# Performance work log

Measured on AMD Instinct MI355X. Metric: run time of the kernel, lower is better.

The kernel has to match this reference:

```python
import jax, jax.numpy as jnp
import numpy as np

N = 50000   # nodes
E = 600000  # edges
IN = 128    # in_channels
H = 128     # hidden
G = 64      # graphs in batch


def setup_inputs() -> dict:
    key = jax.random.key(0)
    ks = jax.random.split(key, 12)
    x = jax.random.normal(ks[0], (N, IN), jnp.float32)
    edge_index = jax.random.randint(ks[1], (2, E), 0, N, dtype=jnp.int64)
    batch = jnp.sort(jax.random.randint(ks[2], (N,), 0, G, dtype=jnp.int64))

    def glorot(k, i, o):
        return jax.random.normal(k, (i, o), jnp.float32) / np.float32(np.sqrt(i))

    return {
        "x": x, "edge_index": edge_index, "batch": batch,
        "W1": glorot(ks[3], IN, H), "b1": jnp.zeros((H,), jnp.float32),
        "W2": glorot(ks[4], H, H),  "b2": jnp.zeros((H,), jnp.float32),
        "W3": glorot(ks[5], H, H),  "b3": jnp.zeros((H,), jnp.float32),
        "Wl": glorot(ks[6], H, 2),  "bl": jnp.zeros((2,), jnp.float32),
    }


def gcn_conv(x, W, b, src, dst, n):
    # PyG GCNConv: linear transform, add self-loops, symmetric deg^-1/2 norm, scatter-add.
    h = x @ W                                   # [n, H]
    loop = jnp.arange(n, dtype=src.dtype)
    s = jnp.concatenate([src, loop])            # [E+n]
    d = jnp.concatenate([dst, loop])
    deg = jax.ops.segment_sum(jnp.ones_like(d, jnp.float32), d, num_segments=n)
    dinv = jax.lax.rsqrt(deg)                   # deg >= 1 thanks to self-loops
    norm = dinv[s] * dinv[d]                    # [E+n]
    out = jax.ops.segment_sum(h[s] * norm[:, None], d, num_segments=n)
    return out + b


def reference(x, edge_index, batch, W1, b1, W2, b2, W3, b3, Wl, bl):
    src, dst = edge_index[0], edge_index[1]
    h = jax.nn.relu(gcn_conv(x, W1, b1, src, dst, N))
    h = jax.nn.relu(gcn_conv(h, W2, b2, src, dst, N))
    h = jax.nn.relu(gcn_conv(h, W3, b3, src, dst, N))
    # global_mean_pool over graph ids
    cnt = jax.ops.segment_sum(jnp.ones((N,), jnp.float32), batch, num_segments=G)
    pooled = jax.ops.segment_sum(h, batch, num_segments=G) / jnp.maximum(cnt, 1.0)[:, None]
    # dropout is identity in eval mode
    return pooled @ Wl + bl                     # [G, 2]
```

## Files before the change

kernel.cpp:

```cpp
#include <hip/hip_runtime.h>


#define THREADS 256
#define ELLW 48
#define ELLS 64

typedef __attribute__((ext_vector_type(8))) short short8;
typedef __attribute__((ext_vector_type(4))) float f32x4;

__device__ inline unsigned short bf16_1(float a) {
    unsigned u = __float_as_uint(a);
    u += 0x7FFF + ((u >> 16) & 1);
    return (unsigned short)(u >> 16);
}
__device__ inline void bf16_split(float f, unsigned short& hi, unsigned short& lo) {
    unsigned u = __float_as_uint(f);
    unsigned r = u + 0x7FFF + ((u >> 16) & 1);
    hi = (unsigned short)(r >> 16);
    float hf = __uint_as_float((unsigned)hi << 16);
    float lf = f - hf;
    unsigned ul = __float_as_uint(lf);
    lo = (unsigned short)((ul + 0x7FFF + ((ul >> 16) & 1)) >> 16);
}

__global__ __launch_bounds__(THREADS) void zero_cnt_k(int* __restrict__ ell, int n) {
    int i = blockIdx.x * THREADS + threadIdx.x;
    if (i < n) ell[(size_t)i * ELLS] = 0;
}

__global__ __launch_bounds__(THREADS) void ell_fill_k(const int* __restrict__ src,
                                                      const int* __restrict__ dst,
                                                      int* __restrict__ ell, int e) {
    int i = blockIdx.x * THREADS + threadIdx.x;
    if (i < e) {
        int d = dst[i];
        int* row = ell + (size_t)d * ELLS;
        int pos = atomicAdd(row, 1);
        if (pos < ELLW) row[1 + pos] = src[i];
    }
}

__global__ __launch_bounds__(THREADS) void dinv_k(const int* __restrict__ ell,
                                                  float* __restrict__ dinv, int n) {
    int i = blockIdx.x * THREADS + threadIdx.x;
    if (i < n) dinv[i] = 1.0f / sqrtf(1.0f + (float)ell[(size_t)i * ELLS]);
}

__global__ void bounds_k(const int* __restrict__ batch, int* __restrict__ gstart,
                         int n, int gtot) {
    int t = threadIdx.x;
    if (t > gtot) return;
    int lo = 0, hi = n;
    while (lo < hi) {
        int mid = (lo + hi) >> 1;
        if (batch[mid] < t) lo = mid + 1; else hi = mid;
    }
    gstart[t] = lo;
}

__global__ __launch_bounds__(THREADS) void wprep_k(const float* __restrict__ W1,
                                                   const float* __restrict__ W2,
                                                   const float* __restrict__ W3,
                                                   unsigned* __restrict__ wf) {
    const float* W = (blockIdx.x == 0) ? W1 : (blockIdx.x == 1) ? W2 : W3;
    unsigned* o_hi = wf + (size_t)blockIdx.x * 16384;
    unsigned* o_lo = o_hi + 8192;
    for (int o = threadIdx.x; o < 8192; o += THREADS) {
        int d = o & 3, l = (o >> 2) & 63, ts = o >> 8;
        int s = ts & 3, t = ts >> 2;
        int k = s * 32 + ((l >> 4) << 3) + d * 2;
        int n = t * 16 + (l & 15);
        float v0 = W[k * 128 + n];
        float v1 = W[(k + 1) * 128 + n];
        unsigned short h0, l0, h1, l1;
        bf16_split(v0, h0, l0);
        bf16_split(v1, h1, l1);
        o_hi[o] = (unsigned)h0 | ((unsigned)h1 << 16);
        o_lo[o] = (unsigned)l0 | ((unsigned)l1 << 16);
    }
}

__global__ __launch_bounds__(THREADS) void mfma_gemm_k(const float* __restrict__ A,
                                                       const unsigned* __restrict__ wf,
                                                       const float* __restrict__ dinv,
                                                       unsigned short* __restrict__ g16u,
                                                       int n) {
    __shared__ unsigned wls[16384];
    int tid = threadIdx.x;
    int lane = tid & 63;
    int r0 = blockIdx.x * 64 + (tid >> 6) * 16;

    for (int i = tid; i < 4096; i += THREADS)
        ((uint4*)wls)[i] = ((const uint4*)wf)[i];

    f32x4 acc[8];
#pragma unroll
    for (int t = 0; t < 8; ++t) acc[t] = (f32x4){0.f, 0.f, 0.f, 0.f};

    int arow = min(r0 + (lane & 15), n - 1);
    const float* ap = A + (size_t)arow * 128 + ((lane >> 4) << 3);

    __syncthreads();

    float4 v0 = *(const float4*)(ap);
    float4 v1 = *(const float4*)(ap + 4);
#pragma unroll
    for (int s = 0; s < 4; ++s) {
        float4 n0, n1;
        if (s < 3) {
            n0 = *(const float4*)(ap + 32 * (s + 1));
            n1 = *(const float4*)(ap + 32 * (s + 1) + 4);
        }
        unsigned short h[8], lo[8];
        bf16_split(v0.x, h[0], lo[0]); bf16_split(v0.y, h[1], lo[1]);
        bf16_split(v0.z, h[2], lo[2]); bf16_split(v0.w, h[3], lo[3]);
        bf16_split(v1.x, h[4], lo[4]); bf16_split(v1.y, h[5], lo[5]);
        bf16_split(v1.z, h[6], lo[6]); bf16_split(v1.w, h[7], lo[7]);
        short8 ah, al;
#pragma unroll
        for (int j = 0; j < 8; ++j) { ah[j] = (short)h[j]; al[j] = (short)lo[j]; }

#pragma unroll
        for (int t = 0; t < 8; ++t) {
            int base = (t * 4 + s) * 256 + lane * 4;
            short8 bh = *(short8*)&wls[base];
            short8 bl = *(short8*)&wls[8192 + base];
            acc[t] = __builtin_amdgcn_mfma_f32_16x16x32_bf16(ah, bh, acc[t], 0, 0, 0);
            acc[t] = __builtin_amdgcn_mfma_f32_16x16x32_bf16(al, bh, acc[t], 0, 0, 0);
            acc[t] = __builtin_amdgcn_mfma_f32_16x16x32_bf16(ah, bl, acc[t], 0, 0, 0);
        }
        v0 = n0; v1 = n1;
    }

    int rbase = r0 + ((lane >> 4) << 2);
    float dv[4];
#pragma unroll
    for (int reg = 0; reg < 4; ++reg) dv[reg] = dinv[min(rbase + reg, n - 1)];
#pragma unroll
    for (int reg = 0; reg < 4; ++reg) {
        int rr = rbase + reg;
        if (rr < n) {
#pragma unroll
            for (int t = 0; t < 8; ++t)
                g16u[(size_t)rr * 128 + t * 16 + (lane & 15)] = bf16_1(acc[t][reg] * dv[reg]);
        }
    }
}

__global__ __launch_bounds__(THREADS) void aggregate_k(const unsigned* __restrict__ g16,
                                                       const int* __restrict__ ell,
                                                       const float* __restrict__ dinv,
                                                       const float* __restrict__ bias,
                                                       float* __restrict__ hout, int n) {
    int wave = (blockIdx.x * THREADS + threadIdx.x) >> 6;
    int lane = threadIdx.x & 63;
    if (wave >= n) return;

    int v = ell[(size_t)wave * ELLS + lane];
    int deg = min(__shfl(v, 0), ELLW);

    unsigned us = g16[(size_t)wave * 64 + lane];
    float ax0 = __uint_as_float(us << 16);
    float ay0 = __uint_as_float(us & 0xFFFF0000u);
    float ax1 = 0.f, ay1 = 0.f, ax2 = 0.f, ay2 = 0.f, ax3 = 0.f, ay3 = 0.f;
    float ax4 = 0.f, ay4 = 0.f, ax5 = 0.f, ay5 = 0.f, ax6 = 0.f, ay6 = 0.f;
    float ax7 = 0.f, ay7 = 0.f;

    for (int k = 0; k < deg; k += 8) {
        int s0 = __shfl(v, k + 1);
        int s1 = __shfl(v, min(k + 2, deg));
        int s2 = __shfl(v, min(k + 3, deg));
        int s3 = __shfl(v, min(k + 4, deg));
        int s4 = __shfl(v, min(k + 5, deg));
        int s5 = __shfl(v, min(k + 6, deg));
        int s6 = __shfl(v, min(k + 7, deg));
        int s7 = __shfl(v, min(k + 8, deg));
        float m1 = (k + 1 < deg) ? 1.f : 0.f;
        float m2 = (k + 2 < deg) ? 1.f : 0.f;
        float m3 = (k + 3 < deg) ? 1.f : 0.f;
        float m4 = (k + 4 < deg) ? 1.f : 0.f;
        float m5 = (k + 5 < deg) ? 1.f : 0.f;
        float m6 = (k + 6 < deg) ? 1.f : 0.f;
        float m7 = (k + 7 < deg) ? 1.f : 0.f;
        unsigned u0 = g16[(size_t)s0 * 64 + lane];
        unsigned u1 = g16[(size_t)s1 * 64 + lane];
        unsigned u2 = g16[(size_t)s2 * 64 + lane];
        unsigned u3 = g16[(size_t)s3 * 64 + lane];
        unsigned u4 = g16[(size_t)s4 * 64 + lane];
        unsigned u5 = g16[(size_t)s5 * 64 + lane];
        unsigned u6 = g16[(size_t)s6 * 64 + lane];
        unsigned u7 = g16[(size_t)s7 * 64 + lane];
        ax0 += __uint_as_float(u0 << 16);
        ay0 += __uint_as_float(u0 & 0xFFFF0000u);
        ax1 = fmaf(m1, __uint_as_float(u1 << 16), ax1);
        ay1 = fmaf(m1, __uint_as_float(u1 & 0xFFFF0000u), ay1);
        ax2 = fmaf(m2, __uint_as_float(u2 << 16), ax2);
        ay2 = fmaf(m2, __uint_as_float(u2 & 0xFFFF0000u), ay2);
        ax3 = fmaf(m3, __uint_as_float(u3 << 16), ax3);
        ay3 = fmaf(m3, __uint_as_float(u3 & 0xFFFF0000u), ay3);
        ax4 = fmaf(m4, __uint_as_float(u4 << 16), ax4);
        ay4 = fmaf(m4, __uint_as_float(u4 & 0xFFFF0000u), ay4);
        ax5 = fmaf(m5, __uint_as_float(u5 << 16), ax5);
        ay5 = fmaf(m5, __uint_as_float(u5 & 0xFFFF0000u), ay5);
        ax6 = fmaf(m6, __uint_as_float(u6 << 16), ax6);
        ay6 = fmaf(m6, __uint_as_float(u6 & 0xFFFF0000u), ay6);
        ax7 = fmaf(m7, __uint_as_float(u7 << 16), ax7);
        ay7 = fmaf(m7, __uint_as_float(u7 & 0xFFFF0000u), ay7);
    }
    ax0 += (ax1 + ax2) + (ax3 + ax4) + (ax5 + ax6) + ax7;
    ay0 += (ay1 + ay2) + (ay3 + ay4) + (ay5 + ay6) + ay7;

    float d = dinv[wave];
    float2 bb = ((const float2*)bias)[lane];
    float2 o;
    o.x = fmaxf(fmaf(d, ax0, bb.x), 0.f);
    o.y = fmaxf(fmaf(d, ay0, bb.y), 0.f);
    ((float2*)hout)[(size_t)wave * 64 + lane] = o;
}

#define PSLICES 8
__global__ __launch_bounds__(THREADS) void pool_k(const float* __restrict__ h,
                                                  const int* __restrict__ gstart,
                                                  float* __restrict__ partial) {
    int gph = blockIdx.x, s = blockIdx.y;
    int start = gstart[gph], end = gstart[gph + 1];
    int len = end - start;
    int chunk = (len + PSLICES - 1) / PSLICES;
    int rs = start + s * chunk;
    int re = min(rs + chunk, end);
    int c = threadIdx.x & 127, half = threadIdx.x >> 7;
    float sum = 0.f;
    for (int r = rs + half; r < re; r += 2) sum += h[r * 128 + c];
    __shared__ float sh[128];
    if (half) sh[c] = sum;
    __syncthreads();
    if (!half) partial[(gph * PSLICES + s) * 128 + c] = sum + sh[c];
}

__global__ __launch_bounds__(128) void final_k(const float* __restrict__ partial,
                                               const int* __restrict__ gstart,
                                               const float* __restrict__ Wl,
                                               const float* __restrict__ bl,
                                               float* __restrict__ out, int gtot) {
    int t = threadIdx.x;
    int gph = t >> 1, j = t & 1;
    if (gph >= gtot) return;
    float cnt = fmaxf((float)(gstart[gph + 1] - gstart[gph]), 1.f);
    float sacc = 0.f;
    for (int k = 0; k < 128; ++k) {
        float v = 0.f;
#pragma unroll
        for (int sb = 0; sb < PSLICES; ++sb)
            v += partial[(gph * PSLICES + sb) * 128 + k];
        sacc = fmaf(v, Wl[k * 2 + j], sacc);
    }
    out[gph * 2 + j] = sacc / cnt + bl[j];
}

extern "C" void kernel_launch(void* const* d_in, const int* in_sizes, int n_in,
                              void* d_out, int out_size, void* d_ws, size_t ws_size,
                              hipStream_t stream) {
    const float* x  = (const float*)d_in[0];
    const int* ei   = (const int*)d_in[1];
    const int* batch= (const int*)d_in[2];
    const float* W1 = (const float*)d_in[3];
    const float* b1 = (const float*)d_in[4];
    const float* W2 = (const float*)d_in[5];
    const float* b2 = (const float*)d_in[6];
    const float* W3 = (const float*)d_in[7];
    const float* b3 = (const float*)d_in[8];
    const float* Wl = (const float*)d_in[9];
    const float* bl = (const float*)d_in[10];
    float* out = (float*)d_out;

    const int N = in_sizes[0] / 128;
    const int E = in_sizes[1] / 2;
    const int G = out_size / 2;
    const int* src = ei;
    const int* dst = ei + E;

    char* ws = (char*)d_ws;
    size_t off = 0;
    auto alloc = [&](size_t bytes) -> void* {
        void* p = ws + off;
        off = (off + bytes + 255) & ~(size_t)255;
        return p;
    };
    unsigned* g16  = (unsigned*)alloc((size_t)N * 64 * 4);
    float* h       = (float*)alloc((size_t)N * 128 * 4);
    float* dinv    = (float*)alloc((size_t)N * 4);
    int* ell       = (int*)alloc((size_t)N * ELLS * 4);
    unsigned* wf   = (unsigned*)alloc((size_t)3 * 16384 * 4);
    float* partial = (float*)alloc((size_t)G * PSLICES * 128 * 4);
    int* gstart    = (int*)alloc((size_t)(G + 1) * 4);
    (void)ws_size;

    int gridE = (E + THREADS - 1) / THREADS;
    int gridN = (N + THREADS - 1) / THREADS;

    zero_cnt_k<<<gridN, THREADS, 0, stream>>>(ell, N);
    wprep_k<<<3, THREADS, 0, stream>>>(W1, W2, W3, wf);
    ell_fill_k<<<gridE, THREADS, 0, stream>>>(src, dst, ell, E);
    dinv_k<<<gridN, THREADS, 0, stream>>>(ell, dinv, N);
    bounds_k<<<1, 128, 0, stream>>>(batch, gstart, N, G);

    int gemmGrid = (N + 63) / 64;
    int aggGrid = (N + 3) / 4;
    unsigned short* g16u = (unsigned short*)g16;

    mfma_gemm_k<<<gemmGrid, THREADS, 0, stream>>>(x, wf, dinv, g16u, N);
    aggregate_k<<<aggGrid, THREADS, 0, stream>>>(g16, ell, dinv, b1, h, N);
    mfma_gemm_k<<<gemmGrid, THREADS, 0, stream>>>(h, wf + 16384, dinv, g16u, N);
    aggregate_k<<<aggGrid, THREADS, 0, stream>>>(g16, ell, dinv, b2, h, N);
    mfma_gemm_k<<<gemmGrid, THREADS, 0, stream>>>(h, wf + 32768, dinv, g16u, N);
    aggregate_k<<<aggGrid, THREADS, 0, stream>>>(g16, ell, dinv, b3, h, N);

    dim3 poolGrid(G, PSLICES);
    pool_k<<<poolGrid, THREADS, 0, stream>>>(h, gstart, partial);
    final_k<<<1, 128, 0, stream>>>(partial, gstart, Wl, bl, out, G);
}
```

Measured before the change: 217.7 us.

## Store hidden activations in bf16, merge prep kernels, compute dinv inline

```diff
diff --git a/kernel.cpp b/kernel.cpp
--- a/kernel.cpp
+++ b/kernel.cpp
@@ -22,10 +22,54 @@
     unsigned ul = __float_as_uint(lf);
     lo = (unsigned short)((ul + 0x7FFF + ((ul >> 16) & 1)) >> 16);
 }
-
-__global__ __launch_bounds__(THREADS) void zero_cnt_k(int* __restrict__ ell, int n) {
-    int i = blockIdx.x * THREADS + threadIdx.x;
-    if (i < n) ell[(size_t)i * ELLS] = 0;
+__device__ inline unsigned pack_bf16(float a, float b) {
+    unsigned ua = __float_as_uint(a);
+    unsigned ub = __float_as_uint(b);
+    ua += 0x7FFF + ((ua >> 16) & 1);
+    ub += 0x7FFF + ((ub >> 16) & 1);
+    return (ua >> 16) | (ub & 0xFFFF0000u);
+}
+
+__global__ __launch_bounds__(THREADS) void prep_k(const float* __restrict__ W1,
+                                                  const float* __restrict__ W2,
+                                                  const float* __restrict__ W3,
+                                                  unsigned* __restrict__ wf,
+                                                  const int* __restrict__ batch,
+                                                  int* __restrict__ gstart,
+                                                  int* __restrict__ ell,
+                                                  int n, int gtot) {
+    int b = blockIdx.x;
+    if (b < 3) {
+        const float* W = (b == 0) ? W1 : (b == 1) ? W2 : W3;
+        unsigned* o_hi = wf + (size_t)b * 16384;
+        unsigned* o_lo = o_hi + 8192;
+        for (int o = threadIdx.x; o < 8192; o += THREADS) {
+            int d = o & 3, l = (o >> 2) & 63, ts = o >> 8;
+            int s = ts & 3, t = ts >> 2;
+            int k = s * 32 + ((l >> 4) << 3) + d * 2;
+            int nn = t * 16 + (l & 15);
+            float v0 = W[k * 128 + nn];
+            float v1 = W[(k + 1) * 128 + nn];
+            unsigned short h0, l0, h1, l1;
+            bf16_split(v0, h0, l0);
+            bf16_split(v1, h1, l1);
+            o_hi[o] = (unsigned)h0 | ((unsigned)h1 << 16);
+            o_lo[o] = (unsigned)l0 | ((unsigned)l1 << 16);
+        }
+    } else if (b == 3) {
+        int t = threadIdx.x;
+        if (t <= gtot) {
+            int lo = 0, hi = n;
+            while (lo < hi) {
+                int mid = (lo + hi) >> 1;
+                if (batch[mid] < t) lo = mid + 1; else hi = mid;
+            }
+            gstart[t] = lo;
+        }
+    } else {
+        int i = (b - 4) * THREADS + threadIdx.x;
+        if (i < n) ell[(size_t)i * ELLS] = 0;
+    }
 }
 
 __global__ __launch_bounds__(THREADS) void ell_fill_k(const int* __restrict__ src,
@@ -40,49 +84,10 @@
     }
 }
 
-__global__ __launch_bounds__(THREADS) void dinv_k(const int* __restrict__ ell,
-                                                  float* __restrict__ dinv, int n) {
-    int i = blockIdx.x * THREADS + threadIdx.x;
-    if (i < n) dinv[i] = 1.0f / sqrtf(1.0f + (float)ell[(size_t)i * ELLS]);
-}
-
-__global__ void bounds_k(const int* __restrict__ batch, int* __restrict__ gstart,
-                         int n, int gtot) {
-    int t = threadIdx.x;
-    if (t > gtot) return;
-    int lo = 0, hi = n;
-    while (lo < hi) {
-        int mid = (lo + hi) >> 1;
-        if (batch[mid] < t) lo = mid + 1; else hi = mid;
-    }
-    gstart[t] = lo;
-}
-
-__global__ __launch_bounds__(THREADS) void wprep_k(const float* __restrict__ W1,
-                                                   const float* __restrict__ W2,
-                                                   const float* __restrict__ W3,
-                                                   unsigned* __restrict__ wf) {
-    const float* W = (blockIdx.x == 0) ? W1 : (blockIdx.x == 1) ? W2 : W3;
-    unsigned* o_hi = wf + (size_t)blockIdx.x * 16384;
-    unsigned* o_lo = o_hi + 8192;
-    for (int o = threadIdx.x; o < 8192; o += THREADS) {
-        int d = o & 3, l = (o >> 2) & 63, ts = o >> 8;
-        int s = ts & 3, t = ts >> 2;
-        int k = s * 32 + ((l >> 4) << 3) + d * 2;
-        int n = t * 16 + (l & 15);
-        float v0 = W[k * 128 + n];
-        float v1 = W[(k + 1) * 128 + n];
-        unsigned short h0, l0, h1, l1;
-        bf16_split(v0, h0, l0);
-        bf16_split(v1, h1, l1);
-        o_hi[o] = (unsigned)h0 | ((unsigned)h1 << 16);
-        o_lo[o] = (unsigned)l0 | ((unsigned)l1 << 16);
-    }
-}
-
-__global__ __launch_bounds__(THREADS) void mfma_gemm_k(const float* __restrict__ A,
+template <bool ABF16>
+__global__ __launch_bounds__(THREADS) void mfma_gemm_k(const void* __restrict__ Av,
                                                        const unsigned* __restrict__ wf,
-                                                       const float* __restrict__ dinv,
+                                                       const int* __restrict__ ell,
                                                        unsigned short* __restrict__ g16u,
                                                        int n) {
     __shared__ unsigned wls[16384];
@@ -98,66 +103,75 @@
     for (int t = 0; t < 8; ++t) acc[t] = (f32x4){0.f, 0.f, 0.f, 0.f};
 
     int arow = min(r0 + (lane & 15), n - 1);
-    const float* ap = A + (size_t)arow * 128 + ((lane >> 4) << 3);
+    int kcol = (lane >> 4) << 3;
+
+    short8 ah[4], al[4];
+    if (ABF16) {
+        const unsigned short* A = (const unsigned short*)Av;
+#pragma unroll
+        for (int s = 0; s < 4; ++s)
+            ah[s] = *(const short8*)&A[(size_t)arow * 128 + kcol + s * 32];
+    } else {
+        const float* A = (const float*)Av;
+        float4 v0[4], v1[4];
+#pragma unroll
+        for (int s = 0; s < 4; ++s) {
+            v0[s] = *(const float4*)&A[(size_t)arow * 128 + kcol + s * 32];
+            v1[s] = *(const float4*)&A[(size_t)arow * 128 + kcol + s * 32 + 4];
+        }
+#pragma unroll
+        for (int s = 0; s < 4; ++s) {
+            unsigned short h[8], lo[8];
+            bf16_split(v0[s].x, h[0], lo[0]); bf16_split(v0[s].y, h[1], lo[1]);
+            bf16_split(v0[s].z, h[2], lo[2]); bf16_split(v0[s].w, h[3], lo[3]);
+            bf16_split(v1[s].x, h[4], lo[4]); bf16_split(v1[s].y, h[5], lo[5]);
+            bf16_split(v1[s].z, h[6], lo[6]); bf16_split(v1[s].w, h[7], lo[7]);
+#pragma unroll
+            for (int j = 0; j < 8; ++j) { ah[s][j] = (short)h[j]; al[s][j] = (short)lo[j]; }
+        }
+    }
 
     __syncthreads();
 
-    float4 v0 = *(const float4*)(ap);
-    float4 v1 = *(const float4*)(ap + 4);
 #pragma unroll
     for (int s = 0; s < 4; ++s) {
-        float4 n0, n1;
-        if (s < 3) {
-            n0 = *(const float4*)(ap + 32 * (s + 1));
-            n1 = *(const float4*)(ap + 32 * (s + 1) + 4);
-        }
-        unsigned short h[8], lo[8];
-        bf16_split(v0.x, h[0], lo[0]); bf16_split(v0.y, h[1], lo[1]);
-        bf16_split(v0.z, h[2], lo[2]); bf16_split(v0.w, h[3], lo[3]);
-        bf16_split(v1.x, h[4], lo[4]); bf16_split(v1.y, h[5], lo[5]);
-        bf16_split(v1.z, h[6], lo[6]); bf16_split(v1.w, h[7], lo[7]);
-        short8 ah, al;
-#pragma unroll
-        for (int j = 0; j < 8; ++j) { ah[j] = (short)h[j]; al[j] = (short)lo[j]; }
-
 #pragma unroll
         for (int t = 0; t < 8; ++t) {
             int base = (t * 4 + s) * 256 + lane * 4;
             short8 bh = *(short8*)&wls[base];
             short8 bl = *(short8*)&wls[8192 + base];
-            acc[t] = __builtin_amdgcn_mfma_f32_16x16x32_bf16(ah, bh, acc[t], 0, 0, 0);
-            acc[t] = __builtin_amdgcn_mfma_f32_16x16x32_bf16(al, bh, acc[t], 0, 0, 0);
-            acc[t] = __builtin_amdgcn_mfma_f32_16x16x32_bf16(ah, bl, acc[t], 0, 0, 0);
-        }
-        v0 = n0; v1 = n1;
+            acc[t] = __builtin_amdgcn_mfma_f32_16x16x32_bf16(ah[s], bh, acc[t], 0, 0, 0);
+            if (!ABF16)
+                acc[t] = __builtin_amdgcn_mfma_f32_16x16x32_bf16(al[s], bh, acc[t], 0, 0, 0);
+            acc[t] = __builtin_amdgcn_mfma_f32_16x16x32_bf16(ah[s], bl, acc[t], 0, 0, 0);
+        }
     }
 
     int rbase = r0 + ((lane >> 4) << 2);
-    float dv[4];
-#pragma unroll
-    for (int reg = 0; reg < 4; ++reg) dv[reg] = dinv[min(rbase + reg, n - 1)];
 #pragma unroll
     for (int reg = 0; reg < 4; ++reg) {
         int rr = rbase + reg;
         if (rr < n) {
+            float dv = rsqrtf(1.f + (float)ell[(size_t)rr * ELLS]);
 #pragma unroll
             for (int t = 0; t < 8; ++t)
-                g16u[(size_t)rr * 128 + t * 16 + (lane & 15)] = bf16_1(acc[t][reg] * dv[reg]);
+                g16u[(size_t)rr * 128 + t * 16 + (lane & 15)] = bf16_1(acc[t][reg] * dv);
         }
     }
 }
 
 __global__ __launch_bounds__(THREADS) void aggregate_k(const unsigned* __restrict__ g16,
                                                        const int* __restrict__ ell,
-                                                       const float* __restrict__ dinv,
                                                        const float* __restrict__ bias,
-                                                       float* __restrict__ hout, int n) {
+                                                       unsigned* __restrict__ h16,
+                                                       int n) {
     int wave = (blockIdx.x * THREADS + threadIdx.x) >> 6;
     int lane = threadIdx.x & 63;
     if (wave >= n) return;
 
     int v = ell[(size_t)wave * ELLS + lane];
-    int deg = min(__shfl(v, 0), ELLW);
+    int cnt_true = __shfl(v, 0);
+    int deg = min(cnt_true, ELLW);
 
     unsigned us = g16[(size_t)wave * 64 + lane];
     float ax0 = __uint_as_float(us << 16);
@@ -210,16 +224,15 @@
     ax0 += (ax1 + ax2) + (ax3 + ax4) + (ax5 + ax6) + ax7;
     ay0 += (ay1 + ay2) + (ay3 + ay4) + (ay5 + ay6) + ay7;
 
-    float d = dinv[wave];
+    float d = rsqrtf(1.f + (float)cnt_true);
     float2 bb = ((const float2*)bias)[lane];
-    float2 o;
-    o.x = fmaxf(fmaf(d, ax0, bb.x), 0.f);
-    o.y = fmaxf(fmaf(d, ay0, bb.y), 0.f);
-    ((float2*)hout)[(size_t)wave * 64 + lane] = o;
+    float ox = fmaxf(fmaf(d, ax0, bb.x), 0.f);
+    float oy = fmaxf(fmaf(d, ay0, bb.y), 0.f);
+    h16[(size_t)wave * 64 + lane] = pack_bf16(ox, oy);
 }
 
 #define PSLICES 8
-__global__ __launch_bounds__(THREADS) void pool_k(const float* __restrict__ h,
+__global__ __launch_bounds__(THREADS) void pool_k(const unsigned* __restrict__ h16,
                                                   const int* __restrict__ gstart,
                                                   float* __restrict__ partial) {
     int gph = blockIdx.x, s = blockIdx.y;
@@ -228,13 +241,23 @@
     int chunk = (len + PSLICES - 1) / PSLICES;
     int rs = start + s * chunk;
     int re = min(rs + chunk, end);
-    int c = threadIdx.x & 127, half = threadIdx.x >> 7;
-    float sum = 0.f;
-    for (int r = rs + half; r < re; r += 2) sum += h[r * 128 + c];
-    __shared__ float sh[128];
-    if (half) sh[c] = sum;
+    int c = threadIdx.x & 63, half = threadIdx.x >> 6;
+    float sx = 0.f, sy = 0.f;
+    for (int r = rs + half; r < re; r += 4) {
+        unsigned u = h16[(size_t)r * 64 + c];
+        sx += __uint_as_float(u << 16);
+        sy += __uint_as_float(u & 0xFFFF0000u);
+    }
+    __shared__ float shx[4][64], shy[4][64];
+    shx[half][c] = sx;
+    shy[half][c] = sy;
     __syncthreads();
-    if (!half) partial[(gph * PSLICES + s) * 128 + c] = sum + sh[c];
+    if (half == 0) {
+        sx = shx[0][c] + shx[1][c] + shx[2][c] + shx[3][c];
+        sy = shy[0][c] + shy[1][c] + shy[2][c] + shy[3][c];
+        partial[(gph * PSLICES + s) * 128 + c * 2] = sx;
+        partial[(gph * PSLICES + s) * 128 + c * 2 + 1] = sy;
+    }
 }
 
 __global__ __launch_bounds__(128) void final_k(const float* __restrict__ partial,
@@ -287,8 +310,7 @@
         return p;
     };
     unsigned* g16  = (unsigned*)alloc((size_t)N * 64 * 4);
-    float* h       = (float*)alloc((size_t)N * 128 * 4);
-    float* dinv    = (float*)alloc((size_t)N * 4);
+    unsigned* h16  = (unsigned*)alloc((size_t)N * 64 * 4);
     int* ell       = (int*)alloc((size_t)N * ELLS * 4);
     unsigned* wf   = (unsigned*)alloc((size_t)3 * 16384 * 4);
     float* partial = (float*)alloc((size_t)G * PSLICES * 128 * 4);
@@ -298,24 +320,21 @@
     int gridE = (E + THREADS - 1) / THREADS;
     int gridN = (N + THREADS - 1) / THREADS;
 
-    zero_cnt_k<<<gridN, THREADS, 0, stream>>>(ell, N);
-    wprep_k<<<3, THREADS, 0, stream>>>(W1, W2, W3, wf);
+    prep_k<<<4 + gridN, THREADS, 0, stream>>>(W1, W2, W3, wf, batch, gstart, ell, N, G);
     ell_fill_k<<<gridE, THREADS, 0, stream>>>(src, dst, ell, E);
-    dinv_k<<<gridN, THREADS, 0, stream>>>(ell, dinv, N);
-    bounds_k<<<1, 128, 0, stream>>>(batch, gstart, N, G);
 
     int gemmGrid = (N + 63) / 64;
     int aggGrid = (N + 3) / 4;
     unsigned short* g16u = (unsigned short*)g16;
 
-    mfma_gemm_k<<<gemmGrid, THREADS, 0, stream>>>(x, wf, dinv, g16u, N);
-    aggregate_k<<<aggGrid, THREADS, 0, stream>>>(g16, ell, dinv, b1, h, N);
-    mfma_gemm_k<<<gemmGrid, THREADS, 0, stream>>>(h, wf + 16384, dinv, g16u, N);
-    aggregate_k<<<aggGrid, THREADS, 0, stream>>>(g16, ell, dinv, b2, h, N);
-    mfma_gemm_k<<<gemmGrid, THREADS, 0, stream>>>(h, wf + 32768, dinv, g16u, N);
-    aggregate_k<<<aggGrid, THREADS, 0, stream>>>(g16, ell, dinv, b3, h, N);
+    mfma_gemm_k<false><<<gemmGrid, THREADS, 0, stream>>>(x, wf, ell, g16u, N);
+    aggregate_k<<<aggGrid, THREADS, 0, stream>>>(g16, ell, b1, h16, N);
+    mfma_gemm_k<true><<<gemmGrid, THREADS, 0, stream>>>(h16, wf + 16384, ell, g16u, N);
+    aggregate_k<<<aggGrid, THREADS, 0, stream>>>(g16, ell, b2, h16, N);
+    mfma_gemm_k<true><<<gemmGrid, THREADS, 0, stream>>>(h16, wf + 32768, ell, g16u, N);
+    aggregate_k<<<aggGrid, THREADS, 0, stream>>>(g16, ell, b3, h16, N);
 
     dim3 poolGrid(G, PSLICES);
-    pool_k<<<poolGrid, THREADS, 0, stream>>>(h, gstart, partial);
+    pool_k<<<poolGrid, THREADS, 0, stream>>>(h16, gstart, partial);
     final_k<<<1, 128, 0, stream>>>(partial, gstart, Wl, bl, out, G);
 }
```

New measurement: 193.9 us. 1.12x faster.
